# Performance work log

Measured on AMD Instinct MI355X. Metric: run time of the kernel, lower is better.

Reference implementation:

```python
import jax, jax.numpy as jnp
import numpy as np

B, C_IN, C_OUT, H, W, K = 8, 64, 64, 128, 128, 3
KK = K * K


def _conv(x, w, b):
    # 3x3, stride 1, padding 1 (matches nn.Conv2d(stride=1, padding=1))
    y = jax.lax.conv_general_dilated(
        x, w, window_strides=(1, 1), padding=((1, 1), (1, 1)),
        dimension_numbers=('NCHW', 'OIHW', 'NCHW'))
    return y + b[None, :, None, None]


def setup_inputs() -> dict:
    key = jax.random.key(0)
    k1, k2, k3, k4, k5 = jax.random.split(key, 5)
    x = jax.random.normal(k1, (B, C_IN, H, W), jnp.float32)
    s = 1.0 / np.sqrt(C_IN * K * K)  # torch conv default init range
    w_off = jax.random.uniform(k2, (2 * KK, C_IN, K, K), jnp.float32, -s, s)
    b_off = jax.random.uniform(k3, (2 * KK,), jnp.float32, -s, s)
    w_reg = jax.random.uniform(k4, (C_OUT, C_IN, K, K), jnp.float32, -s, s)
    b_reg = jax.random.uniform(k5, (C_OUT,), jnp.float32, -s, s)
    return {"x": x, "w_off": w_off, "b_off": b_off, "w_reg": w_reg, "b_reg": b_reg}


def _deform_sample(x, offsets):
    # Equivalent of the K*K grid_sample(align_corners=True, padding_mode='zeros')
    # loop + sum over kernel positions. The norm/unnorm cancel, so sampling is
    # at absolute pixel coords base_grid + offsets.
    B_, C, H_, W_ = x.shape
    off = offsets.reshape(B_, KK, 2, H_, W_).transpose(0, 3, 4, 1, 2)  # B,H,W,KK,2
    xs = off[..., 0] + jnp.arange(W_, dtype=x.dtype)[None, None, :, None]
    ys = off[..., 1] + jnp.arange(H_, dtype=x.dtype)[None, :, None, None]
    x0 = jnp.floor(xs)
    y0 = jnp.floor(ys)
    wx1 = xs - x0
    wx0 = 1.0 - wx1
    wy1 = ys - y0
    wy0 = 1.0 - wy1
    x_flat = x.reshape(B_, C, H_ * W_)

    def gather(yi, xi, w):
        valid = (xi >= 0) & (xi < W_) & (yi >= 0) & (yi < H_)  # zeros padding
        xi_c = jnp.clip(xi, 0, W_ - 1).astype(jnp.int32)
        yi_c = jnp.clip(yi, 0, H_ - 1).astype(jnp.int32)
        idx = (yi_c * W_ + xi_c).reshape(B_, 1, H_ * W_ * KK)
        g = jnp.take_along_axis(
            x_flat, jnp.broadcast_to(idx, (B_, C, H_ * W_ * KK)), axis=2)
        g = g.reshape(B_, C, H_, W_, KK)
        wm = (w * valid.astype(x.dtype))[:, None]  # B,1,H,W,KK
        return (g * wm).sum(-1)  # sum over the KK kernel positions

    return (gather(y0, x0, wy0 * wx0)
            + gather(y0, x0 + 1.0, wy0 * wx1)
            + gather(y0 + 1.0, x0, wy1 * wx0)
            + gather(y0 + 1.0, x0 + 1.0, wy1 * wx1))


def reference(x, w_off, b_off, w_reg, b_reg):
    offsets = _conv(x, w_off, b_off)          # B, 2*KK, H, W
    sampled = _deform_sample(x, offsets)      # B, C, H, W (summed over KK)
    return _conv(sampled, w_reg, b_reg)       # B, C_OUT, H, W
```

## Files before the change

### kernel.cpp

```cpp
#include <hip/hip_runtime.h>

#define B_ 8
#define CIN 64
#define COUT 64
#define H_ 128
#define W_ 128
#define HW (H_*W_)
#define OFFP 24

typedef __attribute__((ext_vector_type(8))) short short8;
typedef __attribute__((ext_vector_type(4))) float f32x4;

__device__ __forceinline__ short f2bf(float f) {
    unsigned u = __float_as_uint(f);
    unsigned r = (u + 0x7fffu + ((u >> 16) & 1u)) >> 16;
    return (short)r;
}
__device__ __forceinline__ float bf2f(short s) {
    return __uint_as_float(((unsigned)(unsigned short)s) << 16);
}

template<int NT>
__device__ __forceinline__ void prep_one(const float* __restrict__ w, short* __restrict__ o,
                                         int i, int n_used) {
    int j = i & 7, lane = (i >> 3) & 63, rest = i >> 9;
    int nt = rest % NT, dc = rest / NT, c = dc & 1, d = dc >> 1;
    int oc = nt * 16 + (lane & 15);
    int ic = c * 32 + (lane >> 4) * 8 + j;
    float v = (oc < n_used) ? w[(oc * 64 + ic) * 9 + d] : 0.f;
    o[i] = f2bf(v);
}

__global__ __launch_bounds__(256) void k_tr(const float* __restrict__ x,
                                            short* __restrict__ xt,
                                            const float* __restrict__ wof,
                                            const float* __restrict__ wrg,
                                            short* __restrict__ wt1,
                                            short* __restrict__ wt2) {
    int i = blockIdx.x * 256 + threadIdx.x;
    if (i < 9 * 2 * 2 * 512) prep_one<2>(wof, wt1, i, 18);
    if (i < 9 * 2 * 4 * 512) prep_one<4>(wrg, wt2, i, 64);

    __shared__ float tile[64 * 129];
    int bh = blockIdx.x;
    int bb = bh & 7, h = bh >> 3;
    const float* xp = x + (size_t)bb * (CIN * HW) + h * W_;
#pragma unroll
    for (int j = 0; j < 32; ++j) {
        int e = threadIdx.x + 256 * j;
        int cc = e >> 7, ww = e & 127;
        tile[cc * 129 + ww] = __builtin_nontemporal_load(xp + cc * HW + ww);
    }
    __syncthreads();
    short* op = xt + (((size_t)(bb << 7) + h) << 13);
#pragma unroll
    for (int j = 0; j < 32; ++j) {
        int e = threadIdx.x + 256 * j;
        int ww = e >> 6, cc = e & 63;
        op[e] = f2bf(tile[cc * 129 + ww]);
    }
}

template<int NT, bool TO_OFF>
__global__ __launch_bounds__(1024, 4) void k_conv(const short* __restrict__ src,
                                                  const short* __restrict__ wt,
                                                  const float* __restrict__ bias,
                                                  short* __restrict__ outb,
                                                  float* __restrict__ outf) {
    __shared__ short At[6 * 130 * 64];
    int blk = blockIdx.x;
    int bb = blk & 7;
    int h0 = (blk >> 3) << 2;

#pragma unroll
    for (int it = 0; it < 7; ++it) {
        int s = threadIdx.x + it * 1024;
        if (s < 6240) {
            int r = s / 1040, rem = s % 1040;
            int px = rem >> 3, ck = rem & 7;
            int y = h0 - 1 + r, xx = px - 1;
            bool v = ((unsigned)y < H_) && ((unsigned)xx < W_);
            int yc = min(max(y, 0), H_ - 1), xc = min(max(xx, 0), W_ - 1);
            short8 val = *(const short8*)(src + ((((size_t)(bb << 7) + yc) << 7) + xc) * 64 + ck * 8);
            short8 z = {0,0,0,0,0,0,0,0};
            if (!v) val = z;
            *(short8*)(&At[(r * 130 + px) * 64 + ((ck ^ (px & 7)) << 3)]) = val;
        }
    }
    __syncthreads();

    int lane = threadIdx.x & 63;
    int wave = threadIdx.x >> 6;
    int lr = wave >> 2;
    int p0 = (wave & 3) * 32;
    int m = lane & 15, quad = lane >> 4;

    f32x4 acc[2][NT];
#pragma unroll
    for (int nt = 0; nt < NT; ++nt) {
        int oc = nt * 16 + m;
        float bv = (!TO_OFF || oc < 18) ? bias[oc] : 0.f;
#pragma unroll
        for (int mt = 0; mt < 2; ++mt) {
            acc[mt][nt][0] = bv; acc[mt][nt][1] = bv;
            acc[mt][nt][2] = bv; acc[mt][nt][3] = bv;
        }
    }

#pragma unroll
    for (int d = 0; d < 9; ++d) {
        int dy = d / 3, dx = d % 3;
#pragma unroll
        for (int c = 0; c < 2; ++c) {
            short8 a[2];
#pragma unroll
            for (int mt = 0; mt < 2; ++mt) {
                int px = p0 + mt * 16 + m + dx;
                a[mt] = *(const short8*)(&At[((lr + dy) * 130 + px) * 64 + (((c * 4 + quad) ^ (px & 7)) << 3)]);
            }
#pragma unroll
            for (int nt = 0; nt < NT; ++nt) {
                short8 b = *(const short8*)(wt + ((((d * 2 + c) * NT + nt) * 64 + lane) << 3));
#pragma unroll
                for (int mt = 0; mt < 2; ++mt)
                    acc[mt][nt] = __builtin_amdgcn_mfma_f32_16x16x32_bf16(a[mt], b, acc[mt][nt], 0, 0, 0);
            }
        }
    }

    if (TO_OFF) {
        __syncthreads();
        unsigned short* St = (unsigned short*)At;
#pragma unroll
        for (int nt = 0; nt < NT; ++nt) {
            int oc = nt * 16 + m;
            if (oc < 20) {
#pragma unroll
                for (int mt = 0; mt < 2; ++mt) {
                    int pl = lr * 128 + p0 + mt * 16 + quad * 4;
#pragma unroll
                    for (int r = 0; r < 4; ++r)
                        St[(pl + r) * OFFP + oc] = (unsigned short)f2bf(acc[mt][nt][r]);
                }
            }
        }
        __syncthreads();
        const unsigned* Sd = (const unsigned*)St;
        unsigned* Od = (unsigned*)(outb + ((size_t)((bb << 14) + (h0 << 7))) * OFFP);
#pragma unroll
        for (int j = 0; j < 6; ++j)
            Od[threadIdx.x + 1024 * j] = Sd[threadIdx.x + 1024 * j];
    } else {
#pragma unroll
        for (int nt = 0; nt < NT; ++nt) {
            int oc = nt * 16 + m;
#pragma unroll
            for (int mt = 0; mt < 2; ++mt) {
                int wpix = p0 + mt * 16 + quad * 4;
                __builtin_nontemporal_store(acc[mt][nt],
                    (f32x4*)(outf + (((size_t)(bb * 64 + oc)) << 14) + ((h0 + lr) << 7) + wpix));
            }
        }
    }
}

__device__ __forceinline__ void prep3(const unsigned* __restrict__ myo, int g,
                                      int w, int h, int cko,
                                      int* __restrict__ eo, float* __restrict__ wg) {
#pragma unroll
    for (int t = 0; t < 3; ++t) {
        unsigned owk = myo[g * 3 + t];
        float ox = bf2f((short)(owk & 0xffff));
        float oy = bf2f((short)(owk >> 16));
        float xs = (float)w + ox, ys = (float)h + oy;
        float x0f = floorf(xs), y0f = floorf(ys);
        float wx1 = xs - x0f, wx0 = 1.f - wx1;
        float wy1 = ys - y0f, wy0 = 1.f - wy1;
        int x0 = (int)x0f, y0 = (int)y0f;
        int x1 = x0 + 1, y1 = y0 + 1;
        int x0c = min(max(x0, 0), W_ - 1), x1c = min(max(x1, 0), W_ - 1);
        int y0c = min(max(y0, 0), H_ - 1), y1c = min(max(y1, 0), H_ - 1);
        bool vx0 = ((unsigned)x0 < W_), vx1 = ((unsigned)x1 < W_);
        bool vy0 = ((unsigned)y0 < H_), vy1 = ((unsigned)y1 < H_);
        wg[t * 4 + 0] = (vy0 && vx0) ? wy0 * wx0 : 0.f;
        wg[t * 4 + 1] = (vy0 && vx1) ? wy0 * wx1 : 0.f;
        wg[t * 4 + 2] = (vy1 && vx0) ? wy1 * wx0 : 0.f;
        wg[t * 4 + 3] = (vy1 && vx1) ? wy1 * wx1 : 0.f;
        eo[t * 4 + 0] = ((y0c * W_ + x0c) << 6) + cko;
        eo[t * 4 + 1] = ((y0c * W_ + x1c) << 6) + cko;
        eo[t * 4 + 2] = ((y1c * W_ + x0c) << 6) + cko;
        eo[t * 4 + 3] = ((y1c * W_ + x1c) << 6) + cko;
    }
}

__global__ __launch_bounds__(256, 2) void k_sample(const short* __restrict__ xt,
                                                   const short* __restrict__ offb,
                                                   short* __restrict__ smp) {
    __shared__ unsigned sow[4 * 96];
    int blk = blockIdx.x;
    int bb = blk & 7;
    int tile = blk >> 3;
    int tw = tile & 15, th = tile >> 4;

    {
        int rowid = threadIdx.x >> 6, rl = threadIdx.x & 63;
        const unsigned* srcp = (const unsigned*)(offb +
            ((size_t)((bb << 14) + (((th << 2) + rowid) << 7) + (tw << 3))) * OFFP);
        sow[rowid * 96 + rl] = srcp[rl];
        if (rl < 32) sow[rowid * 96 + 64 + rl] = srcp[64 + rl];
    }
    __syncthreads();

    int lp = threadIdx.x >> 3;
    int ck = threadIdx.x & 7;
    int w = (tw << 3) + (lp & 7);
    int h = (th << 2) + (lp >> 3);
    int pix = (bb << 14) + (h << 7) + w;
    const short* xim = xt + ((size_t)bb << 20);
    int cko = ck * 8;
    const unsigned* myo = &sow[(lp >> 3) * 96 + (lp & 7) * 12];

    int eoffA[12], eoffB[12];
    float wgtA[12], wgtB[12];
    short8 vA[12], vB[12];
    float acc[8];
#pragma unroll
    for (int i = 0; i < 8; ++i) acc[i] = 0.f;

    prep3(myo, 0, w, h, cko, eoffA, wgtA);
#pragma unroll
    for (int n = 0; n < 12; ++n) vA[n] = *(const short8*)(xim + eoffA[n]);

    prep3(myo, 1, w, h, cko, eoffB, wgtB);
#pragma unroll
    for (int n = 0; n < 12; ++n) vB[n] = *(const short8*)(xim + eoffB[n]);

#pragma unroll
    for (int n = 0; n < 12; ++n) {
        float wv = wgtA[n];
#pragma unroll
        for (int i = 0; i < 8; ++i) acc[i] += wv * bf2f(vA[n][i]);
    }

    prep3(myo, 2, w, h, cko, eoffA, wgtA);
#pragma unroll
    for (int n = 0; n < 12; ++n) vA[n] = *(const short8*)(xim + eoffA[n]);

#pragma unroll
    for (int n = 0; n < 12; ++n) {
        float wv = wgtB[n];
#pragma unroll
        for (int i = 0; i < 8; ++i) acc[i] += wv * bf2f(vB[n][i]);
    }
#pragma unroll
    for (int n = 0; n < 12; ++n) {
        float wv = wgtA[n];
#pragma unroll
        for (int i = 0; i < 8; ++i) acc[i] += wv * bf2f(vA[n][i]);
    }

    short8 o;
#pragma unroll
    for (int i = 0; i < 8; ++i) o[i] = f2bf(acc[i]);
    *(short8*)(smp + (size_t)pix * 64 + cko) = o;
}

extern "C" void kernel_launch(void* const* d_in, const int* in_sizes, int n_in,
                              void* d_out, int out_size, void* d_ws, size_t ws_size,
                              hipStream_t stream) {
    const float* x   = (const float*)d_in[0];
    const float* wof = (const float*)d_in[1];
    const float* bof = (const float*)d_in[2];
    const float* wrg = (const float*)d_in[3];
    const float* brg = (const float*)d_in[4];
    float* out = (float*)d_out;

    char* ws = (char*)d_ws;
    short* xt   = (short*)ws;
    short* smp  = (short*)(ws + 16777216);
    short* offb = (short*)(ws + 2 * 16777216);
    short* wt1  = (short*)(ws + 2 * 16777216 + 6291456);
    short* wt2  = (short*)(ws + 2 * 16777216 + 6291456 + 36864);

    k_tr   <<<dim3(B_ * H_), 256, 0, stream>>>(x, xt, wof, wrg, wt1, wt2);
    k_conv<2, true>  <<<dim3(B_ * H_ / 4), 1024, 0, stream>>>(xt, wt1, bof, offb, nullptr);
    k_sample<<<dim3((B_ * HW * 8) / 256), 256, 0, stream>>>(xt, offb, smp);
    k_conv<4, false> <<<dim3(B_ * H_ / 4), 1024, 0, stream>>>(smp, wt2, brg, nullptr, out);
}
```

Before: 147.5 us.

## Fuse offset convolution with deformable bilinear sampling in one kernel

The offset conv and the deformable sampling are merged into one kernel. Offsets now stay in shared memory instead of a global bf16 buffer, which removes a launch and the global write and read of offsets. Each thread now handles half a pixel's channels in four sequential passes, which lowers the number of gathers in flight per thread compared with the old dedicated sampling kernel. The extra shared memory (about 26KB) may also lower occupancy.

After: 207.7 us. 40.8% more time.

```diff
diff --git a/kernel.cpp b/kernel.cpp
--- a/kernel.cpp
+++ b/kernel.cpp
@@ -6,7 +6,7 @@
 #define H_ 128
 #define W_ 128
 #define HW (H_*W_)
-#define OFFP 24
+#define OFFL 26
 
 typedef __attribute__((ext_vector_type(8))) short short8;
 typedef __attribute__((ext_vector_type(4))) float f32x4;
@@ -61,115 +61,12 @@
     }
 }
 
-template<int NT, bool TO_OFF>
-__global__ __launch_bounds__(1024, 4) void k_conv(const short* __restrict__ src,
-                                                  const short* __restrict__ wt,
-                                                  const float* __restrict__ bias,
-                                                  short* __restrict__ outb,
-                                                  float* __restrict__ outf) {
-    __shared__ short At[6 * 130 * 64];
-    int blk = blockIdx.x;
-    int bb = blk & 7;
-    int h0 = (blk >> 3) << 2;
-
-#pragma unroll
-    for (int it = 0; it < 7; ++it) {
-        int s = threadIdx.x + it * 1024;
-        if (s < 6240) {
-            int r = s / 1040, rem = s % 1040;
-            int px = rem >> 3, ck = rem & 7;
-            int y = h0 - 1 + r, xx = px - 1;
-            bool v = ((unsigned)y < H_) && ((unsigned)xx < W_);
-            int yc = min(max(y, 0), H_ - 1), xc = min(max(xx, 0), W_ - 1);
-            short8 val = *(const short8*)(src + ((((size_t)(bb << 7) + yc) << 7) + xc) * 64 + ck * 8);
-            short8 z = {0,0,0,0,0,0,0,0};
-            if (!v) val = z;
-            *(short8*)(&At[(r * 130 + px) * 64 + ((ck ^ (px & 7)) << 3)]) = val;
-        }
-    }
-    __syncthreads();
-
-    int lane = threadIdx.x & 63;
-    int wave = threadIdx.x >> 6;
-    int lr = wave >> 2;
-    int p0 = (wave & 3) * 32;
-    int m = lane & 15, quad = lane >> 4;
-
-    f32x4 acc[2][NT];
-#pragma unroll
-    for (int nt = 0; nt < NT; ++nt) {
-        int oc = nt * 16 + m;
-        float bv = (!TO_OFF || oc < 18) ? bias[oc] : 0.f;
-#pragma unroll
-        for (int mt = 0; mt < 2; ++mt) {
-            acc[mt][nt][0] = bv; acc[mt][nt][1] = bv;
-            acc[mt][nt][2] = bv; acc[mt][nt][3] = bv;
-        }
-    }
-
-#pragma unroll
-    for (int d = 0; d < 9; ++d) {
-        int dy = d / 3, dx = d % 3;
-#pragma unroll
-        for (int c = 0; c < 2; ++c) {
-            short8 a[2];
-#pragma unroll
-            for (int mt = 0; mt < 2; ++mt) {
-                int px = p0 + mt * 16 + m + dx;
-                a[mt] = *(const short8*)(&At[((lr + dy) * 130 + px) * 64 + (((c * 4 + quad) ^ (px & 7)) << 3)]);
-            }
-#pragma unroll
-            for (int nt = 0; nt < NT; ++nt) {
-                short8 b = *(const short8*)(wt + ((((d * 2 + c) * NT + nt) * 64 + lane) << 3));
-#pragma unroll
-                for (int mt = 0; mt < 2; ++mt)
-                    acc[mt][nt] = __builtin_amdgcn_mfma_f32_16x16x32_bf16(a[mt], b, acc[mt][nt], 0, 0, 0);
-            }
-        }
-    }
-
-    if (TO_OFF) {
-        __syncthreads();
-        unsigned short* St = (unsigned short*)At;
-#pragma unroll
-        for (int nt = 0; nt < NT; ++nt) {
-            int oc = nt * 16 + m;
-            if (oc < 20) {
-#pragma unroll
-                for (int mt = 0; mt < 2; ++mt) {
-                    int pl = lr * 128 + p0 + mt * 16 + quad * 4;
-#pragma unroll
-                    for (int r = 0; r < 4; ++r)
-                        St[(pl + r) * OFFP + oc] = (unsigned short)f2bf(acc[mt][nt][r]);
-                }
-            }
-        }
-        __syncthreads();
-        const unsigned* Sd = (const unsigned*)St;
-        unsigned* Od = (unsigned*)(outb + ((size_t)((bb << 14) + (h0 << 7))) * OFFP);
-#pragma unroll
-        for (int j = 0; j < 6; ++j)
-            Od[threadIdx.x + 1024 * j] = Sd[threadIdx.x + 1024 * j];
-    } else {
-#pragma unroll
-        for (int nt = 0; nt < NT; ++nt) {
-            int oc = nt * 16 + m;
-#pragma unroll
-            for (int mt = 0; mt < 2; ++mt) {
-                int wpix = p0 + mt * 16 + quad * 4;
-                __builtin_nontemporal_store(acc[mt][nt],
-                    (f32x4*)(outf + (((size_t)(bb * 64 + oc)) << 14) + ((h0 + lr) << 7) + wpix));
-            }
-        }
-    }
-}
-
-__device__ __forceinline__ void prep3(const unsigned* __restrict__ myo, int g,
-                                      int w, int h, int cko,
-                                      int* __restrict__ eo, float* __restrict__ wg) {
+__device__ __forceinline__ void prep3w(const unsigned* __restrict__ ow, int g,
+                                       int w, int h, int cko,
+                                       int* __restrict__ eo, float* __restrict__ wg) {
 #pragma unroll
     for (int t = 0; t < 3; ++t) {
-        unsigned owk = myo[g * 3 + t];
+        unsigned owk = ow[g * 3 + t];
         float ox = bf2f((short)(owk & 0xffff));
         float oy = bf2f((short)(owk >> 16));
         float xs = (float)w + ox, ys = (float)h + oy;
@@ -193,76 +90,201 @@
     }
 }
 
-__global__ __launch_bounds__(256, 2) void k_sample(const short* __restrict__ xt,
-                                                   const short* __restrict__ offb,
-                                                   short* __restrict__ smp) {
-    __shared__ unsigned sow[4 * 96];
+__global__ __launch_bounds__(1024, 4) void k_off_sample(const short* __restrict__ xt,
+                                                        const short* __restrict__ wt1,
+                                                        const float* __restrict__ bof,
+                                                        short* __restrict__ smp) {
+    __shared__ short At[6 * 130 * 64];
+    __shared__ unsigned short St[512 * OFFL];
     int blk = blockIdx.x;
     int bb = blk & 7;
-    int tile = blk >> 3;
-    int tw = tile & 15, th = tile >> 4;
+    int h0 = (blk >> 3) << 2;
+
+#pragma unroll
+    for (int it = 0; it < 7; ++it) {
+        int s = threadIdx.x + it * 1024;
+        if (s < 6240) {
+            int r = s / 1040, rem = s % 1040;
+            int px = rem >> 3, ck = rem & 7;
+            int y = h0 - 1 + r, xx = px - 1;
+            bool v = ((unsigned)y < H_) && ((unsigned)xx < W_);
+            int yc = min(max(y, 0), H_ - 1), xc = min(max(xx, 0), W_ - 1);
+            short8 val = *(const short8*)(xt + ((((size_t)(bb << 7) + yc) << 7) + xc) * 64 + ck * 8);
+            short8 z = {0,0,0,0,0,0,0,0};
+            if (!v) val = z;
+            *(short8*)(&At[(r * 130 + px) * 64 + ((ck ^ (px & 7)) << 3)]) = val;
+        }
+    }
+    __syncthreads();
 
     {
-        int rowid = threadIdx.x >> 6, rl = threadIdx.x & 63;
-        const unsigned* srcp = (const unsigned*)(offb +
-            ((size_t)((bb << 14) + (((th << 2) + rowid) << 7) + (tw << 3))) * OFFP);
-        sow[rowid * 96 + rl] = srcp[rl];
-        if (rl < 32) sow[rowid * 96 + 64 + rl] = srcp[64 + rl];
+        int lane = threadIdx.x & 63;
+        int wave = threadIdx.x >> 6;
+        int lr = wave >> 2;
+        int p0 = (wave & 3) * 32;
+        int m = lane & 15, quad = lane >> 4;
+
+        f32x4 acc[2][2];
+#pragma unroll
+        for (int nt = 0; nt < 2; ++nt) {
+            int oc = nt * 16 + m;
+            float bv = (oc < 18) ? bof[oc] : 0.f;
+#pragma unroll
+            for (int mt = 0; mt < 2; ++mt) {
+                acc[mt][nt][0] = bv; acc[mt][nt][1] = bv;
+                acc[mt][nt][2] = bv; acc[mt][nt][3] = bv;
+            }
+        }
+#pragma unroll
+        for (int d = 0; d < 9; ++d) {
+            int dy = d / 3, dx = d % 3;
+#pragma unroll
+            for (int c = 0; c < 2; ++c) {
+                short8 a[2];
+#pragma unroll
+                for (int mt = 0; mt < 2; ++mt) {
+                    int px = p0 + mt * 16 + m + dx;
+                    a[mt] = *(const short8*)(&At[((lr + dy) * 130 + px) * 64 + (((c * 4 + quad) ^ (px & 7)) << 3)]);
+                }
+#pragma unroll
+                for (int nt = 0; nt < 2; ++nt) {
+                    short8 b = *(const short8*)(wt1 + ((((d * 2 + c) * 2 + nt) * 64 + lane) << 3));
+#pragma unroll
+                    for (int mt = 0; mt < 2; ++mt)
+                        acc[mt][nt] = __builtin_amdgcn_mfma_f32_16x16x32_bf16(a[mt], b, acc[mt][nt], 0, 0, 0);
+                }
+            }
+        }
+#pragma unroll
+        for (int nt = 0; nt < 2; ++nt) {
+            int oc = nt * 16 + m;
+            if (oc < 18) {
+#pragma unroll
+                for (int mt = 0; mt < 2; ++mt) {
+                    int pl = lr * 128 + p0 + mt * 16 + quad * 4;
+#pragma unroll
+                    for (int r = 0; r < 4; ++r)
+                        St[(pl + r) * OFFL + oc] = (unsigned short)f2bf(acc[mt][nt][r]);
+                }
+            }
+        }
     }
     __syncthreads();
 
-    int lp = threadIdx.x >> 3;
-    int ck = threadIdx.x & 7;
-    int w = (tw << 3) + (lp & 7);
-    int h = (th << 2) + (lp >> 3);
-    int pix = (bb << 14) + (h << 7) + w;
-    const short* xim = xt + ((size_t)bb << 20);
-    int cko = ck * 8;
-    const unsigned* myo = &sow[(lp >> 3) * 96 + (lp & 7) * 12];
-
-    int eoffA[12], eoffB[12];
-    float wgtA[12], wgtB[12];
-    short8 vA[12], vB[12];
-    float acc[8];
-#pragma unroll
-    for (int i = 0; i < 8; ++i) acc[i] = 0.f;
-
-    prep3(myo, 0, w, h, cko, eoffA, wgtA);
-#pragma unroll
-    for (int n = 0; n < 12; ++n) vA[n] = *(const short8*)(xim + eoffA[n]);
-
-    prep3(myo, 1, w, h, cko, eoffB, wgtB);
-#pragma unroll
-    for (int n = 0; n < 12; ++n) vB[n] = *(const short8*)(xim + eoffB[n]);
-
-#pragma unroll
-    for (int n = 0; n < 12; ++n) {
-        float wv = wgtA[n];
-#pragma unroll
-        for (int i = 0; i < 8; ++i) acc[i] += wv * bf2f(vA[n][i]);
-    }
-
-    prep3(myo, 2, w, h, cko, eoffA, wgtA);
-#pragma unroll
-    for (int n = 0; n < 12; ++n) vA[n] = *(const short8*)(xim + eoffA[n]);
-
-#pragma unroll
-    for (int n = 0; n < 12; ++n) {
-        float wv = wgtB[n];
-#pragma unroll
-        for (int i = 0; i < 8; ++i) acc[i] += wv * bf2f(vB[n][i]);
-    }
-#pragma unroll
-    for (int n = 0; n < 12; ++n) {
-        float wv = wgtA[n];
-#pragma unroll
-        for (int i = 0; i < 8; ++i) acc[i] += wv * bf2f(vA[n][i]);
-    }
-
-    short8 o;
-#pragma unroll
-    for (int i = 0; i < 8; ++i) o[i] = f2bf(acc[i]);
-    *(short8*)(smp + (size_t)pix * 64 + cko) = o;
+    {
+        int t = threadIdx.x;
+        int pxl = t >> 1;
+        int half = t & 1;
+        int w = pxl & 127;
+        int h = h0 + (pxl >> 7);
+        int pix = (bb << 14) + (h << 7) + w;
+        const short* xim = xt + ((size_t)bb << 20);
+
+        unsigned ow[9];
+        const unsigned* myo = (const unsigned*)&St[pxl * OFFL];
+#pragma unroll
+        for (int k = 0; k < 9; ++k) ow[k] = myo[k];
+
+#pragma unroll
+        for (int cq = 0; cq < 4; ++cq) {
+            int cko = ((half << 2) + cq) << 3;
+            float acc[8];
+#pragma unroll
+            for (int i = 0; i < 8; ++i) acc[i] = 0.f;
+#pragma unroll
+            for (int g = 0; g < 3; ++g) {
+                int eo[12]; float wg[12];
+                prep3w(ow, g, w, h, cko, eo, wg);
+                short8 v[12];
+#pragma unroll
+                for (int n = 0; n < 12; ++n) v[n] = *(const short8*)(xim + eo[n]);
+#pragma unroll
+                for (int n = 0; n < 12; ++n) {
+                    float wv = wg[n];
+#pragma unroll
+                    for (int i = 0; i < 8; ++i) acc[i] += wv * bf2f(v[n][i]);
+                }
+            }
+            short8 o;
+#pragma unroll
+            for (int i = 0; i < 8; ++i) o[i] = f2bf(acc[i]);
+            *(short8*)(smp + (size_t)pix * 64 + cko) = o;
+        }
+    }
+}
+
+__global__ __launch_bounds__(1024, 4) void k_conv2(const short* __restrict__ smp,
+                                                   const short* __restrict__ wt2,
+                                                   const float* __restrict__ brg,
+                                                   float* __restrict__ out) {
+    __shared__ short At[6 * 130 * 64];
+    int blk = blockIdx.x;
+    int bb = blk & 7;
+    int h0 = (blk >> 3) << 2;
+
+#pragma unroll
+    for (int it = 0; it < 7; ++it) {
+        int s = threadIdx.x + it * 1024;
+        if (s < 6240) {
+            int r = s / 1040, rem = s % 1040;
+            int px = rem >> 3, ck = rem & 7;
+            int y = h0 - 1 + r, xx = px - 1;
+            bool v = ((unsigned)y < H_) && ((unsigned)xx < W_);
+            int yc = min(max(y, 0), H_ - 1), xc = min(max(xx, 0), W_ - 1);
+            short8 val = *(const short8*)(smp + ((((size_t)(bb << 7) + yc) << 7) + xc) * 64 + ck * 8);
+            short8 z = {0,0,0,0,0,0,0,0};
+            if (!v) val = z;
+            *(short8*)(&At[(r * 130 + px) * 64 + ((ck ^ (px & 7)) << 3)]) = val;
+        }
+    }
+    __syncthreads();
+
+    int lane = threadIdx.x & 63;
+    int wave = threadIdx.x >> 6;
+    int lr = wave >> 2;
+    int p0 = (wave & 3) * 32;
+    int m = lane & 15, quad = lane >> 4;
+
+    f32x4 acc[2][4];
+#pragma unroll
+    for (int nt = 0; nt < 4; ++nt) {
+        float bv = brg[nt * 16 + m];
+#pragma unroll
+        for (int mt = 0; mt < 2; ++mt) {
+            acc[mt][nt][0] = bv; acc[mt][nt][1] = bv;
+            acc[mt][nt][2] = bv; acc[mt][nt][3] = bv;
+        }
+    }
+#pragma unroll
+    for (int d = 0; d < 9; ++d) {
+        int dy = d / 3, dx = d % 3;
+#pragma unroll
+        for (int c = 0; c < 2; ++c) {
+            short8 a[2];
+#pragma unroll
+            for (int mt = 0; mt < 2; ++mt) {
+                int px = p0 + mt * 16 + m + dx;
+                a[mt] = *(const short8*)(&At[((lr + dy) * 130 + px) * 64 + (((c * 4 + quad) ^ (px & 7)) << 3)]);
+            }
+#pragma unroll
+            for (int nt = 0; nt < 4; ++nt) {
+                short8 b = *(const short8*)(wt2 + ((((d * 2 + c) * 4 + nt) * 64 + lane) << 3));
+#pragma unroll
+                for (int mt = 0; mt < 2; ++mt)
+                    acc[mt][nt] = __builtin_amdgcn_mfma_f32_16x16x32_bf16(a[mt], b, acc[mt][nt], 0, 0, 0);
+            }
+        }
+    }
+#pragma unroll
+    for (int nt = 0; nt < 4; ++nt) {
+        int oc = nt * 16 + m;
+#pragma unroll
+        for (int mt = 0; mt < 2; ++mt) {
+            int wpix = p0 + mt * 16 + quad * 4;
+            __builtin_nontemporal_store(acc[mt][nt],
+                (f32x4*)(out + (((size_t)(bb * 64 + oc)) << 14) + ((h0 + lr) << 7) + wpix));
+        }
+    }
 }
 
 extern "C" void kernel_launch(void* const* d_in, const int* in_sizes, int n_in,
@@ -278,12 +300,10 @@
     char* ws = (char*)d_ws;
     short* xt   = (short*)ws;
     short* smp  = (short*)(ws + 16777216);
-    short* offb = (short*)(ws + 2 * 16777216);
-    short* wt1  = (short*)(ws + 2 * 16777216 + 6291456);
-    short* wt2  = (short*)(ws + 2 * 16777216 + 6291456 + 36864);
-
-    k_tr   <<<dim3(B_ * H_), 256, 0, stream>>>(x, xt, wof, wrg, wt1, wt2);
-    k_conv<2, true>  <<<dim3(B_ * H_ / 4), 1024, 0, stream>>>(xt, wt1, bof, offb, nullptr);
-    k_sample<<<dim3((B_ * HW * 8) / 256), 256, 0, stream>>>(xt, offb, smp);
-    k_conv<4, false> <<<dim3(B_ * H_ / 4), 1024, 0, stream>>>(smp, wt2, brg, nullptr, out);
-}
+    short* wt1  = (short*)(ws + 2 * 16777216);
+    short* wt2  = (short*)(ws + 2 * 16777216 + 36864);
+
+    k_tr        <<<dim3(B_ * H_),     256,  0, stream>>>(x, xt, wof, wrg, wt1, wt2);
+    k_off_sample<<<dim3(B_ * H_ / 4), 1024, 0, stream>>>(xt, wt1, bof, smp);
+    k_conv2     <<<dim3(B_ * H_ / 4), 1024, 0, stream>>>(smp, wt2, brg, out);
+}
```
